# Kernel tuning notes

Hardware: AMD Instinct MI355X
Metric: run time of the kernel (lower is better)

## Reference

```python
import jax, jax.numpy as jnp
import numpy as np

LX, LY = 16, 16
N = 2 * LX * LY        # 512 lattice sites (sequence length)
NH = 128               # GRU hidden size
K = 2                  # binary occupation categories
NS = 4096              # number of Monte-Carlo samples (batch)


def setup_inputs() -> dict:
    key = jax.random.key(0)
    k0, k1, k2, k3 = jax.random.split(key, 4)
    gru_kernel = jax.random.normal(k0, (K, 3 * NH), jnp.float32) * (1.0 / np.sqrt(K))
    gru_rkernel = jax.random.normal(k1, (NH, 3 * NH), jnp.float32) * (1.0 / np.sqrt(NH))
    gru_bias = jnp.zeros((2, 3 * NH), jnp.float32)  # [input_bias; recurrent_bias] (reset_after=True)
    dense_w = jax.random.normal(k2, (NH, K), jnp.float32) * (1.0 / np.sqrt(NH))
    dense_b = jnp.zeros((K,), jnp.float32)
    u = jax.random.uniform(k3, (NS, N), jnp.float32)  # pre-drawn noise for categorical draws
    return {"gru_kernel": gru_kernel, "gru_rkernel": gru_rkernel, "gru_bias": gru_bias,
            "dense_w": dense_w, "dense_b": dense_b, "u": u}


def reference(gru_kernel, gru_rkernel, gru_bias, dense_w, dense_b, u):
    """Autoregressive GRU sampling over N lattice sites.
    Returns (samples [ns,N] int32, log_prob [ns] float32)."""
    ns = u.shape[0]
    b_in, b_rec = gru_bias[0], gru_bias[1]

    def step(carry, u_t):
        h, x = carry                       # h: [ns,NH], x: one-hot prev sample [ns,K]
        xg = x @ gru_kernel + b_in          # [ns,3NH]
        hg = h @ gru_rkernel + b_rec        # [ns,3NH]
        xz, xr, xh = jnp.split(xg, 3, axis=-1)   # keras gate order: z, r, h
        hz, hr, hh = jnp.split(hg, 3, axis=-1)
        z = jax.nn.sigmoid(xz + hz)
        r = jax.nn.sigmoid(xr + hr)
        hc = jnp.tanh(xh + r * hh)          # reset_after=True candidate
        h_new = z * h + (1.0 - z) * hc
        probs = jax.nn.softmax(h_new @ dense_w + dense_b, axis=-1)  # [ns,K]
        p1 = probs[:, 1]
        s = (u_t < p1).astype(jnp.int32)    # categorical draw (K=2) via inverse CDF
        logp_t = jnp.log(jnp.where(s == 1, p1, probs[:, 0]) + 1e-10)
        x_new = jax.nn.one_hot(s, K, dtype=h.dtype)
        return (h_new, x_new), (s, logp_t)

    h0 = jnp.zeros((ns, NH), u.dtype)
    x0 = jnp.zeros((ns, K), u.dtype)        # zero input at first site
    (_, _), (samples, logps) = jax.lax.scan(step, (h0, x0), u.T)  # scan over N sites
    return samples.T, logps.sum(axis=0)
```

## Files before the change

kernel.cpp:

```cpp
#include <hip/hip_runtime.h>

#define NHID   128
#define NSTEPS 512
#define NSAMP  4096
#define SPB    16
#define NBLK   256
#define BS     512
#define NWAVE  (BS/64)
#define SAMP_ELEMS (NSAMP * NSTEPS)

__global__ __launch_bounds__(BS, 1)
void vmc_gru_kernel(const float* __restrict__ gk,
                    const float* __restrict__ rk,
                    const float* __restrict__ gb,
                    const float* __restrict__ dw,
                    const float* __restrict__ db,
                    const float* __restrict__ u,
                    float* __restrict__ out)
{
    __shared__ float hsm[NHID * SPB];
    __shared__ float part[NWAVE * SPB * 2];
    __shared__ int   prevs[SPB];

    const int tid = threadIdx.x;
    const int cg  = tid >> 2;
    const int sq  = tid & 3;
    const int s0  = sq * 4;
    const int wv  = tid >> 6;

    for (int i = tid; i < NHID * SPB; i += BS) hsm[i] = 0.0f;
    __syncthreads();

    const float brz = gb[384 + cg];
    const float brr = gb[384 + 128 + cg];
    const float brh = gb[384 + 256 + cg];
    const float xzI = gb[cg],       xz0c = xzI + gk[cg],       xz1c = xzI + gk[384 + cg];
    const float xrI = gb[128 + cg], xr0c = xrI + gk[128 + cg], xr1c = xrI + gk[384 + 128 + cg];
    const float xhI = gb[256 + cg], xh0c = xhI + gk[256 + cg], xh1c = xhI + gk[384 + 256 + cg];
    const float dwc0 = dw[cg * 2], dwc1 = dw[cg * 2 + 1];
    const float db0 = db[0], db1 = db[1];

    const int fsamp = blockIdx.x * SPB + tid;
    float logp = 0.0f;

    for (int t = 0; t < NSTEPS; ++t) {
        float az[4] = {brz, brz, brz, brz};
        float ar[4] = {brr, brr, brr, brr};
        float ah[4] = {brh, brh, brh, brh};
        const float* wp = rk + cg;
        const float* hp = hsm + s0;
        #pragma unroll 4
        for (int k = 0; k < NHID; ++k) {
            const float wz = wp[0];
            const float wr = wp[NHID];
            const float wh = wp[2 * NHID];
            const float4 hv = *(const float4*)hp;
            az[0] = fmaf(wz, hv.x, az[0]); az[1] = fmaf(wz, hv.y, az[1]);
            az[2] = fmaf(wz, hv.z, az[2]); az[3] = fmaf(wz, hv.w, az[3]);
            ar[0] = fmaf(wr, hv.x, ar[0]); ar[1] = fmaf(wr, hv.y, ar[1]);
            ar[2] = fmaf(wr, hv.z, ar[2]); ar[3] = fmaf(wr, hv.w, ar[3]);
            ah[0] = fmaf(wh, hv.x, ah[0]); ah[1] = fmaf(wh, hv.y, ah[1]);
            ah[2] = fmaf(wh, hv.z, ah[2]); ah[3] = fmaf(wh, hv.w, ah[3]);
            wp += 3 * NHID;
            hp += SPB;
        }
        __syncthreads();

        const float4 ho = *(const float4*)(hsm + cg * SPB + s0);
        const int4  pv = *(const int4*)(prevs + s0);
        const float hov[4] = {ho.x, ho.y, ho.z, ho.w};
        const int   pvv[4] = {pv.x, pv.y, pv.z, pv.w};
        float hn[4], p0s[4], p1s[4];
        #pragma unroll
        for (int j = 0; j < 4; ++j) {
            float xz = pvv[j] ? xz1c : xz0c;
            float xr = pvv[j] ? xr1c : xr0c;
            float xh = pvv[j] ? xh1c : xh0c;
            if (t == 0) { xz = xzI; xr = xrI; xh = xhI; }
            const float z  = 1.0f / (1.0f + expf(-(xz + az[j])));
            const float r  = 1.0f / (1.0f + expf(-(xr + ar[j])));
            const float hc = tanhf(xh + r * ah[j]);
            const float hnew = z * hov[j] + (1.0f - z) * hc;
            hn[j] = hnew;
            p0s[j] = hnew * dwc0;
            p1s[j] = hnew * dwc1;
        }
        *(float4*)(hsm + cg * SPB + s0) = make_float4(hn[0], hn[1], hn[2], hn[3]);

        #pragma unroll
        for (int off = 4; off < 64; off <<= 1) {
            #pragma unroll
            for (int j = 0; j < 4; ++j) {
                p0s[j] += __shfl_xor(p0s[j], off);
                p1s[j] += __shfl_xor(p1s[j], off);
            }
        }
        if ((tid & 63) < 4) {
            float* pp = part + wv * (SPB * 2) + s0 * 2;
            #pragma unroll
            for (int j = 0; j < 4; ++j) {
                pp[j * 2 + 0] = p0s[j];
                pp[j * 2 + 1] = p1s[j];
            }
        }
        __syncthreads();

        if (tid < SPB) {
            float l0 = db0, l1 = db1;
            #pragma unroll
            for (int w = 0; w < NWAVE; ++w) {
                const float2 pw = *(const float2*)(part + w * (SPB * 2) + tid * 2);
                l0 += pw.x;
                l1 += pw.y;
            }
            const float mx = fmaxf(l0, l1);
            const float e0 = expf(l0 - mx);
            const float e1 = expf(l1 - mx);
            const float inv = 1.0f / (e0 + e1);
            const float p1 = e1 * inv;
            const float ut = u[(size_t)fsamp * NSTEPS + t];
            const int st = (ut < p1) ? 1 : 0;
            const float psel = st ? p1 : (e0 * inv);
            logp += logf(psel + 1e-10f);
            out[(size_t)fsamp * NSTEPS + t] = (float)st;
            prevs[tid] = st;
        }
    }

    if (tid < SPB) out[SAMP_ELEMS + fsamp] = logp;
}

extern "C" void kernel_launch(void* const* d_in, const int* in_sizes, int n_in,
                              void* d_out, int out_size, void* d_ws, size_t ws_size,
                              hipStream_t stream) {
    const float* gk = (const float*)d_in[0];
    const float* rk = (const float*)d_in[1];
    const float* gb = (const float*)d_in[2];
    const float* dw = (const float*)d_in[3];
    const float* db = (const float*)d_in[4];
    const float* u  = (const float*)d_in[5];
    float* out = (float*)d_out;
    vmc_gru_kernel<<<NBLK, BS, 0, stream>>>(gk, rk, gb, dw, db, u, out);
}
```

Measured before the change: 4.335 ms.

## Split hidden update over 1024 threads with transposed weights and double-buffered h

Doubles the block to 1024 threads so each thread handles one hidden unit for two samples instead of four. The recurrent weights are pre-transposed into workspace so each thread reads contiguous float4 rows, and h is stored sample-major with padding and double-buffered, which removes the mid-step barrier. An extra barrier is added at the end of each step, and the shuffle reduction and partial-sum layout are reworked for 16 waves. The cost is more threads, and so more barrier participants, per block, plus one extra transpose launch before the main kernel.

```diff
diff --git a/kernel.cpp b/kernel.cpp
--- a/kernel.cpp
+++ b/kernel.cpp
@@ -4,31 +4,47 @@
 #define NSTEPS 512
 #define NSAMP  4096
 #define SPB    16
-#define NBLK   256
-#define BS     512
-#define NWAVE  (BS/64)
+#define BS     1024
+#define NBLK   (NSAMP / SPB)
+#define HPAD   132
 #define SAMP_ELEMS (NSAMP * NSTEPS)
+#define WT_ELEMS   (3 * NHID * NHID)
 
-__global__ __launch_bounds__(BS, 1)
+__global__ __launch_bounds__(256)
+void transpose_w_kernel(const float* __restrict__ rk, float* __restrict__ wt) {
+    const int i = blockIdx.x * 256 + threadIdx.x;
+    if (i < WT_ELEMS) {
+        const int c = i / (3 * NHID);
+        const int r = i - c * 3 * NHID;
+        const int g = r >> 7;
+        const int k = r & (NHID - 1);
+        wt[i] = rk[k * 384 + g * NHID + c];
+    }
+}
+
+template<int TR>
+__global__ __launch_bounds__(BS, 4)
 void vmc_gru_kernel(const float* __restrict__ gk,
                     const float* __restrict__ rk,
                     const float* __restrict__ gb,
                     const float* __restrict__ dw,
                     const float* __restrict__ db,
                     const float* __restrict__ u,
+                    const float* __restrict__ wt,
                     float* __restrict__ out)
 {
-    __shared__ float hsm[NHID * SPB];
-    __shared__ float part[NWAVE * SPB * 2];
+    __shared__ float hsm[2][SPB][HPAD];
+    __shared__ float part[16][8][4];
     __shared__ int   prevs[SPB];
 
     const int tid = threadIdx.x;
-    const int cg  = tid >> 2;
-    const int sq  = tid & 3;
-    const int s0  = sq * 4;
+    const int cg  = tid >> 3;
+    const int p   = tid & 7;
+    const int s0  = p * 2;
     const int wv  = tid >> 6;
 
-    for (int i = tid; i < NHID * SPB; i += BS) hsm[i] = 0.0f;
+    for (int i = tid; i < SPB * HPAD; i += BS) (&hsm[0][0][0])[i] = 0.0f;
+    if (tid < SPB) prevs[tid] = 0;
     __syncthreads();
 
     const float brz = gb[384 + cg];
@@ -42,76 +58,105 @@
 
     const int fsamp = blockIdx.x * SPB + tid;
     float logp = 0.0f;
+    int cur = 0;
+
+    const float* wtp = wt + cg * 384;
+    const float* rkp = rk + cg;
 
     for (int t = 0; t < NSTEPS; ++t) {
-        float az[4] = {brz, brz, brz, brz};
-        float ar[4] = {brr, brr, brr, brr};
-        float ah[4] = {brh, brh, brh, brh};
-        const float* wp = rk + cg;
-        const float* hp = hsm + s0;
-        #pragma unroll 4
-        for (int k = 0; k < NHID; ++k) {
-            const float wz = wp[0];
-            const float wr = wp[NHID];
-            const float wh = wp[2 * NHID];
-            const float4 hv = *(const float4*)hp;
-            az[0] = fmaf(wz, hv.x, az[0]); az[1] = fmaf(wz, hv.y, az[1]);
-            az[2] = fmaf(wz, hv.z, az[2]); az[3] = fmaf(wz, hv.w, az[3]);
-            ar[0] = fmaf(wr, hv.x, ar[0]); ar[1] = fmaf(wr, hv.y, ar[1]);
-            ar[2] = fmaf(wr, hv.z, ar[2]); ar[3] = fmaf(wr, hv.w, ar[3]);
-            ah[0] = fmaf(wh, hv.x, ah[0]); ah[1] = fmaf(wh, hv.y, ah[1]);
-            ah[2] = fmaf(wh, hv.z, ah[2]); ah[3] = fmaf(wh, hv.w, ah[3]);
-            wp += 3 * NHID;
-            hp += SPB;
+        float az0 = brz, az1 = brz;
+        float ar0 = brr, ar1 = brr;
+        float ah0 = brh, ah1 = brh;
+        const float* h0p = &hsm[cur][s0][0];
+        const float* h1p = &hsm[cur][s0 + 1][0];
+
+        if (TR) {
+            #pragma unroll 8
+            for (int k4 = 0; k4 < NHID; k4 += 4) {
+                const float4 wz = *(const float4*)(wtp + k4);
+                const float4 wr = *(const float4*)(wtp + 128 + k4);
+                const float4 wh = *(const float4*)(wtp + 256 + k4);
+                const float4 ha = *(const float4*)(h0p + k4);
+                const float4 hb = *(const float4*)(h1p + k4);
+                az0 = fmaf(wz.x, ha.x, az0); az1 = fmaf(wz.x, hb.x, az1);
+                ar0 = fmaf(wr.x, ha.x, ar0); ar1 = fmaf(wr.x, hb.x, ar1);
+                ah0 = fmaf(wh.x, ha.x, ah0); ah1 = fmaf(wh.x, hb.x, ah1);
+                az0 = fmaf(wz.y, ha.y, az0); az1 = fmaf(wz.y, hb.y, az1);
+                ar0 = fmaf(wr.y, ha.y, ar0); ar1 = fmaf(wr.y, hb.y, ar1);
+                ah0 = fmaf(wh.y, ha.y, ah0); ah1 = fmaf(wh.y, hb.y, ah1);
+                az0 = fmaf(wz.z, ha.z, az0); az1 = fmaf(wz.z, hb.z, az1);
+                ar0 = fmaf(wr.z, ha.z, ar0); ar1 = fmaf(wr.z, hb.z, ar1);
+                ah0 = fmaf(wh.z, ha.z, ah0); ah1 = fmaf(wh.z, hb.z, ah1);
+                az0 = fmaf(wz.w, ha.w, az0); az1 = fmaf(wz.w, hb.w, az1);
+                ar0 = fmaf(wr.w, ha.w, ar0); ar1 = fmaf(wr.w, hb.w, ar1);
+                ah0 = fmaf(wh.w, ha.w, ah0); ah1 = fmaf(wh.w, hb.w, ah1);
+            }
+        } else {
+            const float* wp = rkp;
+            #pragma unroll 4
+            for (int k = 0; k < NHID; ++k) {
+                const float wz = wp[0];
+                const float wr = wp[NHID];
+                const float wh = wp[2 * NHID];
+                const float ha = h0p[k];
+                const float hb = h1p[k];
+                az0 = fmaf(wz, ha, az0); az1 = fmaf(wz, hb, az1);
+                ar0 = fmaf(wr, ha, ar0); ar1 = fmaf(wr, hb, ar1);
+                ah0 = fmaf(wh, ha, ah0); ah1 = fmaf(wh, hb, ah1);
+                wp += 3 * NHID;
+            }
         }
-        __syncthreads();
 
-        const float4 ho = *(const float4*)(hsm + cg * SPB + s0);
-        const int4  pv = *(const int4*)(prevs + s0);
-        const float hov[4] = {ho.x, ho.y, ho.z, ho.w};
-        const int   pvv[4] = {pv.x, pv.y, pv.z, pv.w};
-        float hn[4], p0s[4], p1s[4];
-        #pragma unroll
-        for (int j = 0; j < 4; ++j) {
-            float xz = pvv[j] ? xz1c : xz0c;
-            float xr = pvv[j] ? xr1c : xr0c;
-            float xh = pvv[j] ? xh1c : xh0c;
-            if (t == 0) { xz = xzI; xr = xrI; xh = xhI; }
-            const float z  = 1.0f / (1.0f + expf(-(xz + az[j])));
-            const float r  = 1.0f / (1.0f + expf(-(xr + ar[j])));
-            const float hc = tanhf(xh + r * ah[j]);
-            const float hnew = z * hov[j] + (1.0f - z) * hc;
-            hn[j] = hnew;
-            p0s[j] = hnew * dwc0;
-            p1s[j] = hnew * dwc1;
-        }
-        *(float4*)(hsm + cg * SPB + s0) = make_float4(hn[0], hn[1], hn[2], hn[3]);
+        const int pv0 = prevs[s0], pv1 = prevs[s0 + 1];
+        const float ho0 = hsm[cur][s0][cg];
+        const float ho1 = hsm[cur][s0 + 1][cg];
+
+        float xzA = pv0 ? xz1c : xz0c, xzB = pv1 ? xz1c : xz0c;
+        float xrA = pv0 ? xr1c : xr0c, xrB = pv1 ? xr1c : xr0c;
+        float xhA = pv0 ? xh1c : xh0c, xhB = pv1 ? xh1c : xh0c;
+        if (t == 0) { xzA = xzI; xzB = xzI; xrA = xrI; xrB = xrI; xhA = xhI; xhB = xhI; }
+
+        const float zA  = 1.0f / (1.0f + expf(-(xzA + az0)));
+        const float rA  = 1.0f / (1.0f + expf(-(xrA + ar0)));
+        const float hcA = tanhf(xhA + rA * ah0);
+        const float hn0 = zA * ho0 + (1.0f - zA) * hcA;
+
+        const float zB  = 1.0f / (1.0f + expf(-(xzB + az1)));
+        const float rB  = 1.0f / (1.0f + expf(-(xrB + ar1)));
+        const float hcB = tanhf(xhB + rB * ah1);
+        const float hn1 = zB * ho1 + (1.0f - zB) * hcB;
+
+        hsm[cur ^ 1][s0][cg]     = hn0;
+        hsm[cur ^ 1][s0 + 1][cg] = hn1;
+
+        float p00 = hn0 * dwc0, p01 = hn1 * dwc0;
+        float p10 = hn0 * dwc1, p11 = hn1 * dwc1;
 
         #pragma unroll
-        for (int off = 4; off < 64; off <<= 1) {
-            #pragma unroll
-            for (int j = 0; j < 4; ++j) {
-                p0s[j] += __shfl_xor(p0s[j], off);
-                p1s[j] += __shfl_xor(p1s[j], off);
-            }
+        for (int off = 8; off < 64; off <<= 1) {
+            p00 += __shfl_xor(p00, off);
+            p01 += __shfl_xor(p01, off);
+            p10 += __shfl_xor(p10, off);
+            p11 += __shfl_xor(p11, off);
         }
-        if ((tid & 63) < 4) {
-            float* pp = part + wv * (SPB * 2) + s0 * 2;
-            #pragma unroll
-            for (int j = 0; j < 4; ++j) {
-                pp[j * 2 + 0] = p0s[j];
-                pp[j * 2 + 1] = p1s[j];
-            }
+        if ((tid & 63) < 8) {
+            *(float4*)&part[wv][p][0] = make_float4(p00, p01, p10, p11);
         }
         __syncthreads();
 
         if (tid < SPB) {
+            const int sh = tid >> 1, lo = tid & 1;
             float l0 = db0, l1 = db1;
             #pragma unroll
-            for (int w = 0; w < NWAVE; ++w) {
-                const float2 pw = *(const float2*)(part + w * (SPB * 2) + tid * 2);
-                l0 += pw.x;
-                l1 += pw.y;
+            for (int j = 0; j < 8; ++j) {
+                const float4 qa = *(const float4*)&part[2 * j][sh][0];
+                const float4 qb = *(const float4*)&part[2 * j + 1][sh][0];
+                const float a0 = lo ? qa.y : qa.x;
+                const float b0 = lo ? qb.y : qb.x;
+                const float a1 = lo ? qa.w : qa.z;
+                const float b1 = lo ? qb.w : qb.z;
+                l0 += (a0 + b0);
+                l1 += (a1 + b1);
             }
             const float mx = fmaxf(l0, l1);
             const float e0 = expf(l0 - mx);
@@ -125,6 +170,8 @@
             out[(size_t)fsamp * NSTEPS + t] = (float)st;
             prevs[tid] = st;
         }
+        __syncthreads();
+        cur ^= 1;
     }
 
     if (tid < SPB) out[SAMP_ELEMS + fsamp] = logp;
@@ -140,5 +187,12 @@
     const float* db = (const float*)d_in[4];
     const float* u  = (const float*)d_in[5];
     float* out = (float*)d_out;
-    vmc_gru_kernel<<<NBLK, BS, 0, stream>>>(gk, rk, gb, dw, db, u, out);
+
+    if (ws_size >= (size_t)WT_ELEMS * sizeof(float)) {
+        float* wt = (float*)d_ws;
+        transpose_w_kernel<<<(WT_ELEMS + 255) / 256, 256, 0, stream>>>(rk, wt);
+        vmc_gru_kernel<1><<<NBLK, BS, 0, stream>>>(gk, rk, gb, dw, db, u, wt, out);
+    } else {
+        vmc_gru_kernel<0><<<NBLK, BS, 0, stream>>>(gk, rk, gb, dw, db, u, rk, out);
+    }
 }
```

Measured after the change: 6.166 ms. +42.2%, slower.

## Double-buffer hidden state, replicate softmax per thread, preload noise, pack weights

Applied to the files above, without the earlier changes.

Double-buffers the hidden-state and partial-sum shared arrays so each timestep needs one barrier instead of two. Every thread now redundantly finishes the softmax and sampling for its four samples, which removes the serial tid<16 tail and the prevs round trip. The per-block noise slice is staged into shared memory up front. A separate pre-pass repacks the recurrent weights so each thread can fetch them as float4 loads, at the cost of an extra launch and workspace use, with a fallback path when the workspace is too small.

```diff
diff --git a/kernel.cpp b/kernel.cpp
--- a/kernel.cpp
+++ b/kernel.cpp
@@ -4,11 +4,24 @@
 #define NSTEPS 512
 #define NSAMP  4096
 #define SPB    16
-#define NBLK   256
 #define BS     512
-#define NWAVE  (BS/64)
+#define NBLK   (NSAMP / SPB)
 #define SAMP_ELEMS (NSAMP * NSTEPS)
-
+#define WT_ELEMS   (3 * NHID * NHID)
+
+__global__ __launch_bounds__(256)
+void pack_w_kernel(const float* __restrict__ rk, float* __restrict__ wt) {
+    const int i = blockIdx.x * 256 + threadIdx.x;
+    if (i < WT_ELEMS) {
+        const int j  = i & 3;
+        const int c  = (i >> 2) & 127;
+        const int k4 = (i >> 9) & 31;
+        const int g  = i >> 14;
+        wt[i] = rk[(k4 * 4 + j) * 384 + g * NHID + c];
+    }
+}
+
+template<int TR>
 __global__ __launch_bounds__(BS, 1)
 void vmc_gru_kernel(const float* __restrict__ gk,
                     const float* __restrict__ rk,
@@ -16,11 +29,12 @@
                     const float* __restrict__ dw,
                     const float* __restrict__ db,
                     const float* __restrict__ u,
+                    const float* __restrict__ wt,
                     float* __restrict__ out)
 {
-    __shared__ float hsm[NHID * SPB];
-    __shared__ float part[NWAVE * SPB * 2];
-    __shared__ int   prevs[SPB];
+    __shared__ float hsm[2][NHID][SPB];
+    __shared__ float part[2][8][SPB][2];
+    __shared__ float uld[NSTEPS][SPB];
 
     const int tid = threadIdx.x;
     const int cg  = tid >> 2;
@@ -28,7 +42,20 @@
     const int s0  = sq * 4;
     const int wv  = tid >> 6;
 
-    for (int i = tid; i < NHID * SPB; i += BS) hsm[i] = 0.0f;
+    {
+        const int sl = tid >> 5;
+        const int t0 = (tid & 31) * 16;
+        const float* up = u + (size_t)(blockIdx.x * SPB + sl) * NSTEPS + t0;
+        const float4 a = ((const float4*)up)[0];
+        const float4 b = ((const float4*)up)[1];
+        const float4 c = ((const float4*)up)[2];
+        const float4 d = ((const float4*)up)[3];
+        const float tmp[16] = {a.x,a.y,a.z,a.w, b.x,b.y,b.z,b.w,
+                               c.x,c.y,c.z,c.w, d.x,d.y,d.z,d.w};
+        #pragma unroll
+        for (int i = 0; i < 16; ++i) uld[t0 + i][sl] = tmp[i];
+    }
+    for (int i = tid; i < NHID * SPB; i += BS) (&hsm[0][0][0])[i] = 0.0f;
     __syncthreads();
 
     const float brz = gb[384 + cg];
@@ -40,42 +67,86 @@
     const float dwc0 = dw[cg * 2], dwc1 = dw[cg * 2 + 1];
     const float db0 = db[0], db1 = db[1];
 
-    const int fsamp = blockIdx.x * SPB + tid;
-    float logp = 0.0f;
+    const float4* wz4 = (const float4*)wt + cg;
+    const float4* wr4 = (const float4*)wt + 4096 + cg;
+    const float4* wh4 = (const float4*)wt + 8192 + cg;
+    const float* rkp = rk + cg;
+
+    int   pv[4] = {0, 0, 0, 0};
+    float lg[4] = {0.f, 0.f, 0.f, 0.f};
+    int cur = 0;
 
     for (int t = 0; t < NSTEPS; ++t) {
         float az[4] = {brz, brz, brz, brz};
         float ar[4] = {brr, brr, brr, brr};
         float ah[4] = {brh, brh, brh, brh};
-        const float* wp = rk + cg;
-        const float* hp = hsm + s0;
-        #pragma unroll 4
-        for (int k = 0; k < NHID; ++k) {
-            const float wz = wp[0];
-            const float wr = wp[NHID];
-            const float wh = wp[2 * NHID];
-            const float4 hv = *(const float4*)hp;
-            az[0] = fmaf(wz, hv.x, az[0]); az[1] = fmaf(wz, hv.y, az[1]);
-            az[2] = fmaf(wz, hv.z, az[2]); az[3] = fmaf(wz, hv.w, az[3]);
-            ar[0] = fmaf(wr, hv.x, ar[0]); ar[1] = fmaf(wr, hv.y, ar[1]);
-            ar[2] = fmaf(wr, hv.z, ar[2]); ar[3] = fmaf(wr, hv.w, ar[3]);
-            ah[0] = fmaf(wh, hv.x, ah[0]); ah[1] = fmaf(wh, hv.y, ah[1]);
-            ah[2] = fmaf(wh, hv.z, ah[2]); ah[3] = fmaf(wh, hv.w, ah[3]);
-            wp += 3 * NHID;
-            hp += SPB;
-        }
-        __syncthreads();
-
-        const float4 ho = *(const float4*)(hsm + cg * SPB + s0);
-        const int4  pv = *(const int4*)(prevs + s0);
+
+        if (TR) {
+            #pragma unroll 4
+            for (int k4 = 0; k4 < 32; ++k4) {
+                const float4 wz = wz4[k4 * 128];
+                const float4 wr = wr4[k4 * 128];
+                const float4 wh = wh4[k4 * 128];
+                const float4 h0 = *(const float4*)&hsm[cur][4 * k4 + 0][s0];
+                const float4 h1 = *(const float4*)&hsm[cur][4 * k4 + 1][s0];
+                const float4 h2 = *(const float4*)&hsm[cur][4 * k4 + 2][s0];
+                const float4 h3 = *(const float4*)&hsm[cur][4 * k4 + 3][s0];
+                const float hk0[4] = {h0.x, h0.y, h0.z, h0.w};
+                const float hk1[4] = {h1.x, h1.y, h1.z, h1.w};
+                const float hk2[4] = {h2.x, h2.y, h2.z, h2.w};
+                const float hk3[4] = {h3.x, h3.y, h3.z, h3.w};
+                #pragma unroll
+                for (int j = 0; j < 4; ++j) az[j] = fmaf(wz.x, hk0[j], az[j]);
+                #pragma unroll
+                for (int j = 0; j < 4; ++j) ar[j] = fmaf(wr.x, hk0[j], ar[j]);
+                #pragma unroll
+                for (int j = 0; j < 4; ++j) ah[j] = fmaf(wh.x, hk0[j], ah[j]);
+                #pragma unroll
+                for (int j = 0; j < 4; ++j) az[j] = fmaf(wz.y, hk1[j], az[j]);
+                #pragma unroll
+                for (int j = 0; j < 4; ++j) ar[j] = fmaf(wr.y, hk1[j], ar[j]);
+                #pragma unroll
+                for (int j = 0; j < 4; ++j) ah[j] = fmaf(wh.y, hk1[j], ah[j]);
+                #pragma unroll
+                for (int j = 0; j < 4; ++j) az[j] = fmaf(wz.z, hk2[j], az[j]);
+                #pragma unroll
+                for (int j = 0; j < 4; ++j) ar[j] = fmaf(wr.z, hk2[j], ar[j]);
+                #pragma unroll
+                for (int j = 0; j < 4; ++j) ah[j] = fmaf(wh.z, hk2[j], ah[j]);
+                #pragma unroll
+                for (int j = 0; j < 4; ++j) az[j] = fmaf(wz.w, hk3[j], az[j]);
+                #pragma unroll
+                for (int j = 0; j < 4; ++j) ar[j] = fmaf(wr.w, hk3[j], ar[j]);
+                #pragma unroll
+                for (int j = 0; j < 4; ++j) ah[j] = fmaf(wh.w, hk3[j], ah[j]);
+            }
+        } else {
+            const float* wp = rkp;
+            #pragma unroll 4
+            for (int k = 0; k < NHID; ++k) {
+                const float wz = wp[0];
+                const float wr = wp[NHID];
+                const float wh = wp[2 * NHID];
+                const float4 hv = *(const float4*)&hsm[cur][k][s0];
+                const float hk[4] = {hv.x, hv.y, hv.z, hv.w};
+                #pragma unroll
+                for (int j = 0; j < 4; ++j) az[j] = fmaf(wz, hk[j], az[j]);
+                #pragma unroll
+                for (int j = 0; j < 4; ++j) ar[j] = fmaf(wr, hk[j], ar[j]);
+                #pragma unroll
+                for (int j = 0; j < 4; ++j) ah[j] = fmaf(wh, hk[j], ah[j]);
+                wp += 3 * NHID;
+            }
+        }
+
+        const float4 ho = *(const float4*)&hsm[cur][cg][s0];
         const float hov[4] = {ho.x, ho.y, ho.z, ho.w};
-        const int   pvv[4] = {pv.x, pv.y, pv.z, pv.w};
         float hn[4], p0s[4], p1s[4];
         #pragma unroll
         for (int j = 0; j < 4; ++j) {
-            float xz = pvv[j] ? xz1c : xz0c;
-            float xr = pvv[j] ? xr1c : xr0c;
-            float xh = pvv[j] ? xh1c : xh0c;
+            float xz = pv[j] ? xz1c : xz0c;
+            float xr = pv[j] ? xr1c : xr0c;
+            float xh = pv[j] ? xh1c : xh0c;
             if (t == 0) { xz = xzI; xr = xrI; xh = xhI; }
             const float z  = 1.0f / (1.0f + expf(-(xz + az[j])));
             const float r  = 1.0f / (1.0f + expf(-(xr + ar[j])));
@@ -85,7 +156,7 @@
             p0s[j] = hnew * dwc0;
             p1s[j] = hnew * dwc1;
         }
-        *(float4*)(hsm + cg * SPB + s0) = make_float4(hn[0], hn[1], hn[2], hn[3]);
+        *(float4*)&hsm[cur ^ 1][cg][s0] = make_float4(hn[0], hn[1], hn[2], hn[3]);
 
         #pragma unroll
         for (int off = 4; off < 64; off <<= 1) {
@@ -95,39 +166,48 @@
                 p1s[j] += __shfl_xor(p1s[j], off);
             }
         }
+        const int pb = t & 1;
         if ((tid & 63) < 4) {
-            float* pp = part + wv * (SPB * 2) + s0 * 2;
-            #pragma unroll
-            for (int j = 0; j < 4; ++j) {
-                pp[j * 2 + 0] = p0s[j];
-                pp[j * 2 + 1] = p1s[j];
-            }
+            *(float4*)&part[pb][wv][s0][0]     = make_float4(p0s[0], p1s[0], p0s[1], p1s[1]);
+            *(float4*)&part[pb][wv][s0 + 2][0] = make_float4(p0s[2], p1s[2], p0s[3], p1s[3]);
         }
         __syncthreads();
 
-        if (tid < SPB) {
-            float l0 = db0, l1 = db1;
-            #pragma unroll
-            for (int w = 0; w < NWAVE; ++w) {
-                const float2 pw = *(const float2*)(part + w * (SPB * 2) + tid * 2);
-                l0 += pw.x;
-                l1 += pw.y;
-            }
-            const float mx = fmaxf(l0, l1);
-            const float e0 = expf(l0 - mx);
-            const float e1 = expf(l1 - mx);
+        float l0[4] = {db0, db0, db0, db0};
+        float l1[4] = {db1, db1, db1, db1};
+        #pragma unroll
+        for (int w = 0; w < 8; ++w) {
+            const float4 qa = *(const float4*)&part[pb][w][s0][0];
+            const float4 qb = *(const float4*)&part[pb][w][s0 + 2][0];
+            l0[0] += qa.x; l1[0] += qa.y;
+            l0[1] += qa.z; l1[1] += qa.w;
+            l0[2] += qb.x; l1[2] += qb.y;
+            l0[3] += qb.z; l1[3] += qb.w;
+        }
+        const float4 uu = *(const float4*)&uld[t][s0];
+        const float uv[4] = {uu.x, uu.y, uu.z, uu.w};
+        #pragma unroll
+        for (int j = 0; j < 4; ++j) {
+            const float mx = fmaxf(l0[j], l1[j]);
+            const float e0 = expf(l0[j] - mx);
+            const float e1 = expf(l1[j] - mx);
             const float inv = 1.0f / (e0 + e1);
-            const float p1 = e1 * inv;
-            const float ut = u[(size_t)fsamp * NSTEPS + t];
-            const int st = (ut < p1) ? 1 : 0;
-            const float psel = st ? p1 : (e0 * inv);
-            logp += logf(psel + 1e-10f);
-            out[(size_t)fsamp * NSTEPS + t] = (float)st;
-            prevs[tid] = st;
-        }
-    }
-
-    if (tid < SPB) out[SAMP_ELEMS + fsamp] = logp;
+            const float p1v = e1 * inv;
+            const int st = (uv[j] < p1v) ? 1 : 0;
+            const float psel = st ? p1v : (e0 * inv);
+            lg[j] += logf(psel + 1e-10f);
+            pv[j] = st;
+            if (cg == 0)
+                out[(size_t)(blockIdx.x * SPB + s0 + j) * NSTEPS + t] = (float)st;
+        }
+        cur ^= 1;
+    }
+
+    if (cg == 0) {
+        #pragma unroll
+        for (int j = 0; j < 4; ++j)
+            out[SAMP_ELEMS + blockIdx.x * SPB + s0 + j] = lg[j];
+    }
 }
 
 extern "C" void kernel_launch(void* const* d_in, const int* in_sizes, int n_in,
@@ -140,5 +220,12 @@
     const float* db = (const float*)d_in[4];
     const float* u  = (const float*)d_in[5];
     float* out = (float*)d_out;
-    vmc_gru_kernel<<<NBLK, BS, 0, stream>>>(gk, rk, gb, dw, db, u, out);
+
+    if (ws_size >= (size_t)WT_ELEMS * sizeof(float)) {
+        float* wt = (float*)d_ws;
+        pack_w_kernel<<<(WT_ELEMS + 255) / 256, 256, 0, stream>>>(rk, wt);
+        vmc_gru_kernel<1><<<NBLK, BS, 0, stream>>>(gk, rk, gb, dw, db, u, wt, out);
+    } else {
+        vmc_gru_kernel<0><<<NBLK, BS, 0, stream>>>(gk, rk, gb, dw, db, u, rk, out);
+    }
 }
```

After: 4.440 ms. 1.02x slower.
